# Performance work log

Hardware: AMD Instinct MI355X
Metric: run time of the kernel (lower is better)

The kernel has to match this reference:

```python
import jax, jax.numpy as jnp
import numpy as np

N_HEAD = 16
N_KV_HEAD = 8
HEAD_DIM = 128
N_EMBED = 2048
EPS = 1.1920929e-07  # torch default eps for fp32 rms_norm


def _apply_rotary_emb(x, cos, sin):
    # x: (B, T, H, D); cos/sin: (1, T, 1, D//2)  (nanochat-style half rotation)
    d = x.shape[-1] // 2
    x1, x2 = x[..., :d], x[..., d:]
    y1 = x1 * cos + x2 * sin
    y2 = -x1 * sin + x2 * cos
    return jnp.concatenate([y1, y2], axis=-1).astype(x.dtype)


def _rms_norm(x):
    return x * jax.lax.rsqrt(jnp.mean(jnp.square(x), axis=-1, keepdims=True) + EPS)


def setup_inputs() -> dict:
    key = jax.random.key(0)
    ks = jax.random.split(key, 5)
    B, T = 2, 2048
    kv_dim = N_KV_HEAD * HEAD_DIM
    x = jax.random.normal(ks[0], (B, T, N_EMBED), dtype=jnp.float32)
    w_attn = jax.random.normal(ks[1], (N_EMBED + 2 * kv_dim, N_EMBED), dtype=jnp.float32) * 0.02
    w_proj = jax.random.normal(ks[2], (N_EMBED, N_EMBED), dtype=jnp.float32) * 0.02
    # realistic RoPE tables
    half = HEAD_DIM // 2
    inv_freq = 1.0 / (10000.0 ** (jnp.arange(half, dtype=jnp.float32) / half))
    freqs = jnp.arange(T, dtype=jnp.float32)[:, None] * inv_freq[None, :]  # (T, half)
    cos = jnp.cos(freqs)[None, :, None, :]
    sin = jnp.sin(freqs)[None, :, None, :]
    return {"x": x, "w_attn": w_attn, "w_proj": w_proj, "cos": cos, "sin": sin}


def reference(x, w_attn, w_proj, cos, sin):
    B, T, C = x.shape
    kv_dim = N_KV_HEAD * HEAD_DIM
    qkv = jnp.einsum('btc,oc->bto', x, w_attn)  # (B, T, C + 2*kv_dim)
    q = qkv[..., :C].reshape(B, T, N_HEAD, HEAD_DIM)
    k = qkv[..., C:C + kv_dim].reshape(B, T, N_KV_HEAD, HEAD_DIM)
    v = qkv[..., C + kv_dim:].reshape(B, T, N_KV_HEAD, HEAD_DIM)
    q = _rms_norm(_apply_rotary_emb(q, cos, sin))
    k = _rms_norm(_apply_rotary_emb(k, cos, sin))
    # GQA: repeat kv heads to match query heads
    rep = N_HEAD // N_KV_HEAD
    k = jnp.repeat(k, rep, axis=2)  # (B, T, n_head, D)
    v = jnp.repeat(v, rep, axis=2)
    scale = 1.0 / jnp.sqrt(jnp.float32(HEAD_DIM))
    scores = jnp.einsum('bqhd,bkhd->bhqk', q, k) * scale  # (B, H, T, T)
    causal = jnp.tril(jnp.ones((T, T), dtype=bool))
    scores = jnp.where(causal[None, None], scores, jnp.finfo(scores.dtype).min)
    attn = jax.nn.softmax(scores, axis=-1)
    y = jnp.einsum('bhqk,bkhd->bqhd', attn, v).reshape(B, T, C)
    return jnp.einsum('btc,oc->bto', y, w_proj)
```

## Files before the change

kernel.cpp:

```cpp
#include <hip/hip_runtime.h>

#define B_ 2
#define T_ 2048
#define NH 16
#define NKV 8
#define HD 128
#define C_ 2048
#define KVD (NKV*HD)
#define QKVD (C_ + 2*KVD)
#define NTOK (B_*T_)

typedef __bf16 bf16_t;
typedef __bf16 bf16x2_t __attribute__((ext_vector_type(2)));
typedef __bf16 bf16x4_t __attribute__((ext_vector_type(4)));
typedef __bf16 bf16x8_t __attribute__((ext_vector_type(8)));
typedef float f32x4_t __attribute__((ext_vector_type(4)));
typedef float f32x16_t __attribute__((ext_vector_type(16)));
typedef int i32x4_t __attribute__((ext_vector_type(4)));

__device__ __forceinline__ f32x4_t mfma16(bf16x8_t a, bf16x8_t b, f32x4_t c) {
  return __builtin_amdgcn_mfma_f32_16x16x32_bf16(a, b, c, 0, 0, 0);
}
__device__ __forceinline__ f32x16_t mfma32(bf16x8_t a, bf16x8_t b, f32x16_t c) {
  return __builtin_amdgcn_mfma_f32_32x32x16_bf16(a, b, c, 0, 0, 0);
}
__device__ __forceinline__ f32x16_t zero16() {
  f32x16_t z;
  #pragma unroll
  for (int i = 0; i < 16; i++) z[i] = 0.f;
  return z;
}
__device__ __forceinline__ int pk2(float a, float b) {
  bf16x2_t t; t[0] = (bf16_t)a; t[1] = (bf16_t)b;
  return __builtin_bit_cast(int, t);
}

#define GLDS16(gp, lp) __builtin_amdgcn_global_load_lds( \
    (const __attribute__((address_space(1))) void*)(gp), \
    (__attribute__((address_space(3))) void*)(lp), 16, 0, 0)

__global__ __launch_bounds__(256) void cvt3_kernel(const float* __restrict__ s0, bf16_t* __restrict__ d0,
                                                   const float* __restrict__ s1, bf16_t* __restrict__ d1,
                                                   const float* __restrict__ s2, bf16_t* __restrict__ d2) {
  int bid = blockIdx.x;
  const float* s; bf16_t* d; int off;
  if (bid < 8192)       { s = s0; d = d0; off = bid; }
  else if (bid < 16384) { s = s1; d = d1; off = bid - 8192; }
  else                  { s = s2; d = d2; off = bid - 16384; }
  int i = (off * 256 + threadIdx.x) * 4;
  const float4 v = *(const float4*)(s + i);
  bf16x4_t o;
  o[0] = (bf16_t)v.x; o[1] = (bf16_t)v.y; o[2] = (bf16_t)v.z; o[3] = (bf16_t)v.w;
  *(bf16x4_t*)(d + i) = o;
}

__global__ void gemm_nt(const bf16_t* __restrict__ A, const bf16_t* __restrict__ Bm,
                        float* __restrict__ Cf, bf16_t* __restrict__ Cb, int M, int N, int K) {
  __shared__ bf16_t As[128*32];
  __shared__ bf16_t Bs[128*32];
  int tid = threadIdx.x;
  int wave = tid >> 6, lane = tid & 63;
  int quad = lane >> 4, l16 = lane & 15;
  int wm = (wave >> 1) * 64, wn = (wave & 1) * 64;
  int bm = blockIdx.y * 128, bn = blockIdx.x * 128;
  int grow = wave * 32 + (lane >> 2);
  int gcol = (lane & 3) * 8;
  const bf16_t* pa = A + (size_t)(bm + grow) * K + gcol;
  const bf16_t* pb = Bm + (size_t)(bn + grow) * K + gcol;
  bf16_t* lA0 = &As[(wave * 32) * 32];
  bf16_t* lA1 = &As[(wave * 32 + 16) * 32];
  bf16_t* lB0 = &Bs[(wave * 32) * 32];
  bf16_t* lB1 = &Bs[(wave * 32 + 16) * 32];
  f32x4_t acc[4][4];
  #pragma unroll
  for (int i = 0; i < 4; i++)
    #pragma unroll
    for (int j = 0; j < 4; j++) acc[i][j] = (f32x4_t){0.f,0.f,0.f,0.f};
  for (int k0 = 0; k0 < K; k0 += 32) {
    __syncthreads();
    GLDS16(pa + k0, lA0);
    GLDS16(pa + (size_t)16 * K + k0, lA1);
    GLDS16(pb + k0, lB0);
    GLDS16(pb + (size_t)16 * K + k0, lB1);
    __syncthreads();
    bf16x8_t af[4], bfr[4];
    #pragma unroll
    for (int i = 0; i < 4; i++) {
      af[i]  = *(const bf16x8_t*)&As[(wm + i*16 + l16)*32 + quad*8];
      bfr[i] = *(const bf16x8_t*)&Bs[(wn + i*16 + l16)*32 + quad*8];
    }
    #pragma unroll
    for (int i = 0; i < 4; i++)
      #pragma unroll
      for (int j = 0; j < 4; j++)
        acc[i][j] = mfma16(af[i], bfr[j], acc[i][j]);
  }
  if (Cb) {
    #pragma unroll
    for (int i = 0; i < 4; i++)
      #pragma unroll
      for (int j = 0; j < 4; j++) {
        int row0 = bm + wm + i*16 + quad*4;
        int col  = bn + wn + j*16 + l16;
        #pragma unroll
        for (int r = 0; r < 4; r++)
          Cb[(size_t)(row0 + r) * N + col] = (bf16_t)acc[i][j][r];
      }
  } else {
    #pragma unroll
    for (int i = 0; i < 4; i++)
      #pragma unroll
      for (int j = 0; j < 4; j++) {
        int row0 = bm + wm + i*16 + quad*4;
        int col  = bn + wn + j*16 + l16;
        #pragma unroll
        for (int r = 0; r < 4; r++)
          Cf[(size_t)(row0 + r) * N + col] = acc[i][j][r];
      }
  }
}

__global__ __launch_bounds__(256) void rope_norm_kernel(const bf16_t* __restrict__ qkv,
    const float* __restrict__ cosb, const float* __restrict__ sinb,
    bf16_t* __restrict__ qb, bf16_t* __restrict__ kb) {
  int token = blockIdx.y;
  int slot = blockIdx.x * 4 + (threadIdx.x >> 6);
  int lane = threadIdx.x & 63;
  int b = token >> 11, s = token & 2047;
  const bf16_t* row = qkv + (size_t)token * QKVD;
  int base_in = (slot < 16) ? slot * HD : C_ + (slot - 16) * HD;
  float x1 = (float)row[base_in + lane];
  float x2 = (float)row[base_in + 64 + lane];
  float c = cosb[s*64 + lane], sn = sinb[s*64 + lane];
  float y1 = x1*c + x2*sn;
  float y2 = x2*c - x1*sn;
  float ss = y1*y1 + y2*y2;
  ss += __shfl_xor(ss, 1);  ss += __shfl_xor(ss, 2);  ss += __shfl_xor(ss, 4);
  ss += __shfl_xor(ss, 8);  ss += __shfl_xor(ss, 16); ss += __shfl_xor(ss, 32);
  float r = rsqrtf(ss * (1.0f/128.0f) + 1.1920929e-07f);
  bf16_t* dst;
  if (slot < 16) {
    r *= 0.08838834764831845f * 1.4426950408889634f;
    dst = qb + ((size_t)(b*NH + slot) * T_ + s) * HD;
  } else {
    dst = kb + ((size_t)(b*NKV + (slot-16)) * T_ + s) * HD;
  }
  dst[lane]      = (bf16_t)(y1 * r);
  dst[lane + 64] = (bf16_t)(y2 * r);
}

__global__ __launch_bounds__(256) void transpose_v(const bf16_t* __restrict__ qkv,
                                                   bf16_t* __restrict__ vt) {
  __shared__ bf16_t TT[64*136];
  int bk = blockIdx.y;
  int b = bk >> 3, kv = bk & 7;
  int s0 = blockIdx.x * 64;
  int tid = threadIdx.x;
  int row = tid >> 2, c0 = (tid & 3) * 32;
  const bf16_t* src = qkv + (size_t)(b*T_ + s0 + row) * QKVD + C_ + KVD + kv*HD + c0;
  #pragma unroll
  for (int s4 = 0; s4 < 4; s4++)
    *(bf16x8_t*)&TT[row*136 + c0 + s4*8] = *(const bf16x8_t*)(src + s4*8);
  __syncthreads();
  #pragma unroll
  for (int s2 = 0; s2 < 2; s2++) {
    int d = (tid >> 2) + s2*64;
    #pragma unroll
    for (int s = 0; s < 2; s++) {
      int g = (tid & 3) * 8 + s*32;
      bf16x8_t pk;
      #pragma unroll
      for (int e = 0; e < 8; e++) pk[e] = TT[(g + e)*136 + d];
      *(bf16x8_t*)(vt + ((size_t)bk * HD + d) * T_ + s0 + g) = pk;
    }
  }
}

__global__ __launch_bounds__(256, 2) void attn_kernel(const bf16_t* __restrict__ qb,
    const bf16_t* __restrict__ kb, const bf16_t* __restrict__ vt, bf16_t* __restrict__ yb) {
  __shared__ bf16_t Ksb[2][64*136];
  __shared__ bf16_t Vsb[2][128*72];
  int L = blockIdx.x;
  int bh = L & 31;
  int qt = 15 - (L >> 5);
  int b = bh >> 4, h = bh & 15, kvh = h >> 1;
  int tid = threadIdx.x, wave = tid >> 6, lane = tid & 63;
  int l32 = lane & 31, half = lane >> 5;
  const bf16_t* Qp = qb + (size_t)bh * T_ * HD;
  const bf16_t* Kp = kb + (size_t)(b*NKV + kvh) * T_ * HD;
  const bf16_t* Vt = vt + (size_t)(b*NKV + kvh) * HD * T_;

  int krow = tid >> 2, kcb = (tid & 3) * 32;
  int vd = tid >> 1,  vcb = (tid & 1) * 32;

  int qrow = qt*128 + wave*32 + l32;
  bf16x8_t qf[8];
  #pragma unroll
  for (int kc = 0; kc < 8; kc++)
    qf[kc] = *(const bf16x8_t*)(Qp + (size_t)qrow * HD + kc*16 + half*8);

  float mrow = -1e30f, lrow = 0.f;
  f32x16_t o[4];
  #pragma unroll
  for (int mb = 0; mb < 4; mb++) o[mb] = zero16();

  int nkt = 2*qt + 2;
  bf16x8_t kreg[4], vreg[4];
  {
    const bf16_t* srck = Kp + (size_t)krow * HD + kcb;
    const bf16_t* srcv = Vt + (size_t)vd * T_ + vcb;
    #pragma unroll
    for (int s2 = 0; s2 < 4; s2++) { kreg[s2] = *(const bf16x8_t*)(srck + s2*8);
                                     vreg[s2] = *(const bf16x8_t*)(srcv + s2*8); }
  }
  #pragma unroll
  for (int s2 = 0; s2 < 4; s2++) { *(bf16x8_t*)&Ksb[0][krow*136 + kcb + s2*8] = kreg[s2];
                                   *(bf16x8_t*)&Vsb[0][vd*72   + vcb + s2*8] = vreg[s2]; }

  for (int kt = 0; kt < nkt; kt++) {
    __syncthreads();
    int cur = kt & 1;
    if (kt + 1 < nkt) {
      int k1 = (kt + 1) * 64;
      const bf16_t* srck = Kp + (size_t)(k1 + krow) * HD + kcb;
      const bf16_t* srcv = Vt + (size_t)vd * T_ + k1 + vcb;
      #pragma unroll
      for (int s2 = 0; s2 < 4; s2++) { kreg[s2] = *(const bf16x8_t*)(srck + s2*8);
                                       vreg[s2] = *(const bf16x8_t*)(srcv + s2*8); }
    }
    int k0 = kt * 64;
    f32x16_t sacc[2];
    sacc[0] = zero16(); sacc[1] = zero16();
    #pragma unroll
    for (int kc = 0; kc < 8; kc++)
      #pragma unroll
      for (int mb = 0; mb < 2; mb++) {
        bf16x8_t kf = *(const bf16x8_t*)&Ksb[cur][(mb*32 + l32)*136 + kc*16 + half*8];
        sacc[mb] = mfma32(kf, qf[kc], sacc[mb]);
      }
    if (k0 + 63 > qt*128 + wave*32) {
      #pragma unroll
      for (int mb = 0; mb < 2; mb++)
        #pragma unroll
        for (int r = 0; r < 16; r++) {
          int key = k0 + mb*32 + (r&3) + 8*(r>>2) + 4*half;
          if (key > qrow) sacc[mb][r] = -1e30f;
        }
    }
    float mx = -1e30f;
    #pragma unroll
    for (int mb = 0; mb < 2; mb++)
      #pragma unroll
      for (int r = 0; r < 16; r++) mx = fmaxf(mx, sacc[mb][r]);
    mx = fmaxf(mx, __shfl_xor(mx, 32));
    float mnew = fmaxf(mrow, mx);
    float alpha = exp2f(mrow - mnew);
    mrow = mnew;
    float rs = 0.f;
    #pragma unroll
    for (int mb = 0; mb < 2; mb++)
      #pragma unroll
      for (int r = 0; r < 16; r++) {
        float p = exp2f(sacc[mb][r] - mnew);
        sacc[mb][r] = p;
        rs += p;
      }
    rs += __shfl_xor(rs, 32);
    lrow = lrow * alpha + rs;
    #pragma unroll
    for (int mb = 0; mb < 4; mb++) o[mb] = o[mb] * alpha;
    int P2[2][4][2];
    #pragma unroll
    for (int mb = 0; mb < 2; mb++)
      #pragma unroll
      for (int g = 0; g < 4; g++) {
        P2[mb][g][0] = pk2(sacc[mb][4*g+0], sacc[mb][4*g+1]);
        P2[mb][g][1] = pk2(sacc[mb][4*g+2], sacc[mb][4*g+3]);
      }
    #pragma unroll
    for (int kc = 0; kc < 4; kc++) {
      int mb = kc >> 1, c = kc & 1;
      int o0 = half ? P2[mb][2*c+1][0] : P2[mb][2*c][0];
      int o1 = half ? P2[mb][2*c+1][1] : P2[mb][2*c][1];
      int s0 = half ? P2[mb][2*c][0]   : P2[mb][2*c+1][0];
      int s1 = half ? P2[mb][2*c][1]   : P2[mb][2*c+1][1];
      int r0 = __shfl_xor(s0, 32);
      int r1 = __shfl_xor(s1, 32);
      i32x4_t wv;
      wv[0] = half ? r0 : o0;
      wv[1] = half ? r1 : o1;
      wv[2] = half ? o0 : r0;
      wv[3] = half ? o1 : r1;
      bf16x8_t pf = __builtin_bit_cast(bf16x8_t, wv);
      #pragma unroll
      for (int mbd = 0; mbd < 4; mbd++) {
        bf16x8_t vf = *(const bf16x8_t*)&Vsb[cur][(mbd*32 + l32)*72 + kc*16 + half*8];
        o[mbd] = mfma32(vf, pf, o[mbd]);
      }
    }
    if (kt + 1 < nkt) {
      #pragma unroll
      for (int s2 = 0; s2 < 4; s2++) { *(bf16x8_t*)&Ksb[1-cur][krow*136 + kcb + s2*8] = kreg[s2];
                                       *(bf16x8_t*)&Vsb[1-cur][vd*72   + vcb + s2*8] = vreg[s2]; }
    }
  }
  __syncthreads();
  bf16_t* OL = (wave < 2) ? &Ksb[0][wave * 4352] : &Ksb[1][(wave - 2) * 4352];
  float invl = 1.0f / lrow;
  #pragma unroll
  for (int mb = 0; mb < 4; mb++)
    #pragma unroll
    for (int rr = 0; rr < 4; rr++) {
      bf16x4_t pk;
      pk[0] = (bf16_t)(o[mb][rr*4+0] * invl); pk[1] = (bf16_t)(o[mb][rr*4+1] * invl);
      pk[2] = (bf16_t)(o[mb][rr*4+2] * invl); pk[3] = (bf16_t)(o[mb][rr*4+3] * invl);
      *(bf16x4_t*)&OL[l32*136 + mb*32 + rr*8 + half*4] = pk;
    }
  int tok = qt*128 + wave*32 + l32;
  bf16_t* dst = yb + ((size_t)(b*T_ + tok) * NH + h) * HD + half*64;
  #pragma unroll
  for (int jj = 0; jj < 8; jj++)
    *(bf16x8_t*)(dst + jj*8) = *(const bf16x8_t*)&OL[l32*136 + half*64 + jj*8];
}

extern "C" void kernel_launch(void* const* d_in, const int* in_sizes, int n_in,
                              void* d_out, int out_size, void* d_ws, size_t ws_size,
                              hipStream_t stream) {
  const float* x      = (const float*)d_in[0];
  const float* w_attn = (const float*)d_in[1];
  const float* w_proj = (const float*)d_in[2];
  const float* cosb   = (const float*)d_in[3];
  const float* sinb   = (const float*)d_in[4];
  float* out = (float*)d_out;

  bf16_t* xb   = (bf16_t*)d_ws;
  bf16_t* wab  = xb + 8388608;
  bf16_t* wpb  = wab + 8388608;
  bf16_t* qkvb = wpb + 4194304;
  bf16_t* qb   = qkvb + 16777216;
  bf16_t* kb   = qb + 8388608;
  bf16_t* vt   = kb + 4194304;
  bf16_t* yb   = vt + 4194304;

  cvt3_kernel<<<20480, 256, 0, stream>>>(x, xb, w_attn, wab, w_proj, wpb);

  gemm_nt<<<dim3(32, 32), 256, 0, stream>>>(xb, wab, nullptr, qkvb, NTOK, QKVD, C_);

  rope_norm_kernel<<<dim3(6, 4096), 256, 0, stream>>>(qkvb, cosb, sinb, qb, kb);
  transpose_v<<<dim3(32, 16), 256, 0, stream>>>(qkvb, vt);

  attn_kernel<<<512, 256, 0, stream>>>(qb, kb, vt, yb);

  gemm_nt<<<dim3(16, 32), 256, 0, stream>>>(yb, wpb, out, nullptr, NTOK, C_, C_);
}
```

Measured before the change: 340.0 us.

## Split attention KV range across two wave groups per block and merge partials

Doubles the attention block to 512 threads. Two groups of four waves each process half of the causal key tiles for the same 128-query tile, each with its own double-buffered K/V shared memory. At the end, group 1 writes its partial output, max and sum to shared memory, and group 0 merges them with log-sum-exp rescaling before writing. This shortens the serial key loop per block to cut the tail latency of long causal tiles. The costs are higher shared-memory use, one block per CU, and an extra merge step.

```diff
diff --git a/kernel.cpp b/kernel.cpp
--- a/kernel.cpp
+++ b/kernel.cpp
@@ -176,24 +176,32 @@
   }
 }
 
-__global__ __launch_bounds__(256, 2) void attn_kernel(const bf16_t* __restrict__ qb,
+__global__ __launch_bounds__(512, 1) void attn_kernel(const bf16_t* __restrict__ qb,
     const bf16_t* __restrict__ kb, const bf16_t* __restrict__ vt, bf16_t* __restrict__ yb) {
-  __shared__ bf16_t Ksb[2][64*136];
-  __shared__ bf16_t Vsb[2][128*72];
+  __shared__ __align__(16) bf16_t Ks[2][2][64*136];
+  __shared__ __align__(16) bf16_t Vs[2][2][128*72];
   int L = blockIdx.x;
   int bh = L & 31;
   int qt = 15 - (L >> 5);
   int b = bh >> 4, h = bh & 15, kvh = h >> 1;
-  int tid = threadIdx.x, wave = tid >> 6, lane = tid & 63;
+  int tid = threadIdx.x;
+  int wv = tid >> 6;
+  int g  = wv >> 2;
+  int sq = wv & 3;
+  int lane = tid & 63;
   int l32 = lane & 31, half = lane >> 5;
+  int t256 = tid & 255;
   const bf16_t* Qp = qb + (size_t)bh * T_ * HD;
   const bf16_t* Kp = kb + (size_t)(b*NKV + kvh) * T_ * HD;
   const bf16_t* Vt = vt + (size_t)(b*NKV + kvh) * HD * T_;
 
-  int krow = tid >> 2, kcb = (tid & 3) * 32;
-  int vd = tid >> 1,  vcb = (tid & 1) * 32;
-
-  int qrow = qt*128 + wave*32 + l32;
+  int krow = t256 >> 2, kcb = (t256 & 3) * 32;
+  int vd = t256 >> 1,  vcb = (t256 & 1) * 32;
+
+  int h0 = qt + 1;
+  int kt0 = g * h0;
+
+  int qrow = qt*128 + sq*32 + l32;
   bf16x8_t qf[8];
   #pragma unroll
   for (int kc = 0; kc < 8; kc++)
@@ -204,41 +212,40 @@
   #pragma unroll
   for (int mb = 0; mb < 4; mb++) o[mb] = zero16();
 
-  int nkt = 2*qt + 2;
   bf16x8_t kreg[4], vreg[4];
   {
-    const bf16_t* srck = Kp + (size_t)krow * HD + kcb;
-    const bf16_t* srcv = Vt + (size_t)vd * T_ + vcb;
+    const bf16_t* srck = Kp + (size_t)(kt0*64 + krow) * HD + kcb;
+    const bf16_t* srcv = Vt + (size_t)vd * T_ + kt0*64 + vcb;
     #pragma unroll
     for (int s2 = 0; s2 < 4; s2++) { kreg[s2] = *(const bf16x8_t*)(srck + s2*8);
                                      vreg[s2] = *(const bf16x8_t*)(srcv + s2*8); }
   }
   #pragma unroll
-  for (int s2 = 0; s2 < 4; s2++) { *(bf16x8_t*)&Ksb[0][krow*136 + kcb + s2*8] = kreg[s2];
-                                   *(bf16x8_t*)&Vsb[0][vd*72   + vcb + s2*8] = vreg[s2]; }
-
-  for (int kt = 0; kt < nkt; kt++) {
+  for (int s2 = 0; s2 < 4; s2++) { *(bf16x8_t*)&Ks[g][0][krow*136 + kcb + s2*8] = kreg[s2];
+                                   *(bf16x8_t*)&Vs[g][0][vd*72   + vcb + s2*8] = vreg[s2]; }
+
+  for (int t = 0; t < h0; t++) {
     __syncthreads();
-    int cur = kt & 1;
-    if (kt + 1 < nkt) {
-      int k1 = (kt + 1) * 64;
+    int cur = t & 1;
+    if (t + 1 < h0) {
+      int k1 = (kt0 + t + 1) * 64;
       const bf16_t* srck = Kp + (size_t)(k1 + krow) * HD + kcb;
       const bf16_t* srcv = Vt + (size_t)vd * T_ + k1 + vcb;
       #pragma unroll
       for (int s2 = 0; s2 < 4; s2++) { kreg[s2] = *(const bf16x8_t*)(srck + s2*8);
                                        vreg[s2] = *(const bf16x8_t*)(srcv + s2*8); }
     }
-    int k0 = kt * 64;
+    int k0 = (kt0 + t) * 64;
     f32x16_t sacc[2];
     sacc[0] = zero16(); sacc[1] = zero16();
     #pragma unroll
     for (int kc = 0; kc < 8; kc++)
       #pragma unroll
       for (int mb = 0; mb < 2; mb++) {
-        bf16x8_t kf = *(const bf16x8_t*)&Ksb[cur][(mb*32 + l32)*136 + kc*16 + half*8];
+        bf16x8_t kf = *(const bf16x8_t*)&Ks[g][cur][(mb*32 + l32)*136 + kc*16 + half*8];
         sacc[mb] = mfma32(kf, qf[kc], sacc[mb]);
       }
-    if (k0 + 63 > qt*128 + wave*32) {
+    if (k0 + 63 > qt*128 + sq*32) {
       #pragma unroll
       for (int mb = 0; mb < 2; mb++)
         #pragma unroll
@@ -273,9 +280,9 @@
     #pragma unroll
     for (int mb = 0; mb < 2; mb++)
       #pragma unroll
-      for (int g = 0; g < 4; g++) {
-        P2[mb][g][0] = pk2(sacc[mb][4*g+0], sacc[mb][4*g+1]);
-        P2[mb][g][1] = pk2(sacc[mb][4*g+2], sacc[mb][4*g+3]);
+      for (int gg = 0; gg < 4; gg++) {
+        P2[mb][gg][0] = pk2(sacc[mb][4*gg+0], sacc[mb][4*gg+1]);
+        P2[mb][gg][1] = pk2(sacc[mb][4*gg+2], sacc[mb][4*gg+3]);
       }
     #pragma unroll
     for (int kc = 0; kc < 4; kc++) {
@@ -286,41 +293,59 @@
       int s1 = half ? P2[mb][2*c][1]   : P2[mb][2*c+1][1];
       int r0 = __shfl_xor(s0, 32);
       int r1 = __shfl_xor(s1, 32);
-      i32x4_t wv;
-      wv[0] = half ? r0 : o0;
-      wv[1] = half ? r1 : o1;
-      wv[2] = half ? o0 : r0;
-      wv[3] = half ? o1 : r1;
-      bf16x8_t pf = __builtin_bit_cast(bf16x8_t, wv);
+      i32x4_t wvv;
+      wvv[0] = half ? r0 : o0;
+      wvv[1] = half ? r1 : o1;
+      wvv[2] = half ? o0 : r0;
+      wvv[3] = half ? o1 : r1;
+      bf16x8_t pf = __builtin_bit_cast(bf16x8_t, wvv);
       #pragma unroll
       for (int mbd = 0; mbd < 4; mbd++) {
-        bf16x8_t vf = *(const bf16x8_t*)&Vsb[cur][(mbd*32 + l32)*72 + kc*16 + half*8];
+        bf16x8_t vf = *(const bf16x8_t*)&Vs[g][cur][(mbd*32 + l32)*72 + kc*16 + half*8];
         o[mbd] = mfma32(vf, pf, o[mbd]);
       }
     }
-    if (kt + 1 < nkt) {
-      #pragma unroll
-      for (int s2 = 0; s2 < 4; s2++) { *(bf16x8_t*)&Ksb[1-cur][krow*136 + kcb + s2*8] = kreg[s2];
-                                       *(bf16x8_t*)&Vsb[1-cur][vd*72   + vcb + s2*8] = vreg[s2]; }
+    if (t + 1 < h0) {
+      #pragma unroll
+      for (int s2 = 0; s2 < 4; s2++) { *(bf16x8_t*)&Ks[g][1-cur][krow*136 + kcb + s2*8] = kreg[s2];
+                                       *(bf16x8_t*)&Vs[g][1-cur][vd*72   + vcb + s2*8] = vreg[s2]; }
     }
   }
   __syncthreads();
-  bf16_t* OL = (wave < 2) ? &Ksb[0][wave * 4352] : &Ksb[1][(wave - 2) * 4352];
-  float invl = 1.0f / lrow;
-  #pragma unroll
-  for (int mb = 0; mb < 4; mb++)
-    #pragma unroll
-    for (int rr = 0; rr < 4; rr++) {
-      bf16x4_t pk;
-      pk[0] = (bf16_t)(o[mb][rr*4+0] * invl); pk[1] = (bf16_t)(o[mb][rr*4+1] * invl);
-      pk[2] = (bf16_t)(o[mb][rr*4+2] * invl); pk[3] = (bf16_t)(o[mb][rr*4+3] * invl);
-      *(bf16x4_t*)&OL[l32*136 + mb*32 + rr*8 + half*4] = pk;
-    }
-  int tok = qt*128 + wave*32 + l32;
-  bf16_t* dst = yb + ((size_t)(b*T_ + tok) * NH + h) * HD + half*64;
-  #pragma unroll
-  for (int jj = 0; jj < 8; jj++)
-    *(bf16x8_t*)(dst + jj*8) = *(const bf16x8_t*)&OL[l32*136 + half*64 + jj*8];
+  float* MG = (float*)Vs;
+  int mbase = (sq*64 + lane) * 66;
+  if (g == 1) {
+    #pragma unroll
+    for (int mb = 0; mb < 4; mb++)
+      #pragma unroll
+      for (int r = 0; r < 16; r++) MG[mbase + mb*16 + r] = o[mb][r];
+    MG[mbase + 64] = mrow;
+    MG[mbase + 65] = lrow;
+  }
+  __syncthreads();
+  if (g == 0) {
+    float m1 = MG[mbase + 64], l1v = MG[mbase + 65];
+    float mm = fmaxf(mrow, m1);
+    float a0 = exp2f(mrow - mm), a1 = exp2f(m1 - mm);
+    float invl = 1.0f / (lrow * a0 + l1v * a1);
+    a0 *= invl; a1 *= invl;
+    bf16_t* OL = &((bf16_t*)Ks)[sq * 4352];
+    #pragma unroll
+    for (int mb = 0; mb < 4; mb++)
+      #pragma unroll
+      for (int rr = 0; rr < 4; rr++) {
+        bf16x4_t pk;
+        #pragma unroll
+        for (int jj = 0; jj < 4; jj++)
+          pk[jj] = (bf16_t)(o[mb][rr*4+jj] * a0 + MG[mbase + mb*16 + rr*4 + jj] * a1);
+        *(bf16x4_t*)&OL[l32*136 + mb*32 + rr*8 + half*4] = pk;
+      }
+    int tok = qt*128 + sq*32 + l32;
+    bf16_t* dst = yb + ((size_t)(b*T_ + tok) * NH + h) * HD + half*64;
+    #pragma unroll
+    for (int jj = 0; jj < 8; jj++)
+      *(bf16x8_t*)(dst + jj*8) = *(const bf16x8_t*)&OL[l32*136 + half*64 + jj*8];
+  }
 }
 
 extern "C" void kernel_launch(void* const* d_in, const int* in_sizes, int n_in,
@@ -349,7 +374,7 @@
   rope_norm_kernel<<<dim3(6, 4096), 256, 0, stream>>>(qkvb, cosb, sinb, qb, kb);
   transpose_v<<<dim3(32, 16), 256, 0, stream>>>(qkvb, vt);
 
-  attn_kernel<<<512, 256, 0, stream>>>(qb, kb, vt, yb);
+  attn_kernel<<<512, 512, 0, stream>>>(qb, kb, vt, yb);
 
   gemm_nt<<<dim3(16, 32), 256, 0, stream>>>(yb, wpb, out, nullptr, NTOK, C_, C_);
 }
```

After: 335.8 us. No clear change (-1.2%).
